# Optimization experiments

Measured on AMD Instinct MI355X. Metric: run time of the kernel, lower is better.

The kernel has to match this reference:

```python
import jax, jax.numpy as jnp
import numpy as np

LAMBDA = 0.5
WINDOW = 2
NUM_SCALES = 2
EPS = 1e-5


def setup_inputs() -> dict:
    key = jax.random.key(0)
    ks = jax.random.split(key, 9)
    N, C, T, Vw = 32, 96, 300, 50
    V = 25
    out_c = 192
    return {
        "x": jax.random.normal(ks[0], (N, C, T, Vw), jnp.float32),
        "xx": jax.random.normal(ks[1], (N, 3, 300, V), jnp.float32),
        "A_res": jax.random.normal(ks[2], (Vw, Vw), jnp.float32) * 1e-6,
        "W": jax.random.normal(ks[3], (out_c, NUM_SCALES * C), jnp.float32) * 0.05,
        "b": jax.random.normal(ks[4], (out_c,), jnp.float32) * 0.01,
        "gamma": jnp.ones((out_c,), jnp.float32),
        "beta": jnp.zeros((out_c,), jnp.float32),
        "running_mean": jax.random.normal(ks[5], (out_c,), jnp.float32) * 0.01,
        "running_var": jax.random.uniform(ks[6], (out_c,), jnp.float32, 0.5, 1.5),
    }


def reference(x, xx, A_res, W, b, gamma, beta, running_mean, running_var):
    # xx: (N, 3, 300, V) -> (N, T=300, V, C=3)
    xxp = jnp.transpose(xx, (0, 2, 3, 1))
    # pairwise squared L2 distances (norm then squared in exp == sum of squares)
    diff = xxp[:, :, :, None, :] - xxp[:, :, None, :, :]      # (N,T,V,V,3)
    dists2 = jnp.sum(diff * diff, axis=-1)                     # (N,T,V,V)
    A_dsg = jnp.exp(-dists2 / LAMBDA)
    # conv3d with (1,1,300,1,1) kernel of 1/300 == mean over the 300 frames
    A_t = jnp.mean(A_dsg, axis=1)                              # (N,V,V)
    # per-sample symmetric normalization D^-1/2 A D^-1/2
    deg = jnp.sum(A_t, axis=-1)                                # (N,V)
    dinv = deg ** -0.5
    A_norm = A_t * dinv[:, :, None] * dinv[:, None, :]
    # kron-style repeat to spatial-temporal graph (N, V*window, V*window)
    A_large = jnp.tile(A_norm, (1, WINDOW, WINDOW))
    A = A_large + A_res                                        # (N,Vw,Vw)
    # conv2d with (1,N,1,1) kernel of 1/N == mean over the batch
    A_scale = jnp.mean(A, axis=0)                              # (Vw,Vw)
    # graph conv
    agg = jnp.einsum('vu,nctu->nctv', A_scale, x)              # (N,C,T,Vw)
    N, C, T, Vw = x.shape
    Vs = Vw // NUM_SCALES
    agg = agg.reshape(N, C, T, NUM_SCALES, Vs)
    agg = jnp.transpose(agg, (0, 3, 1, 2, 4)).reshape(N, NUM_SCALES * C, T, Vs)
    # MLP: 1x1 conv + BN (activation='linear')
    out = jnp.einsum('oc,nctv->notv', W, agg) + b[None, :, None, None]
    scale = gamma * jax.lax.rsqrt(running_var + EPS)
    out = out * scale[None, :, None, None] + (beta - running_mean * scale)[None, :, None, None]
    return jax.nn.relu(out)
```

## Files before the change

### kernel.cpp

```cpp
#include <hip/hip_runtime.h>
#include <hip/hip_bf16.h>

typedef __attribute__((ext_vector_type(8))) short short8;
typedef __attribute__((ext_vector_type(4))) short short4v;
typedef __attribute__((ext_vector_type(4))) float f32x4;
typedef __attribute__((ext_vector_type(2))) float f32x2;

__device__ __forceinline__ unsigned short f2bf(float f) {
    unsigned int u = __builtin_bit_cast(unsigned int, f);
    u += 0x7fffu + ((u >> 16) & 1u);
    return (unsigned short)(u >> 16);
}
__device__ __forceinline__ unsigned int pack2(float a, float b) {
    union { __hip_bfloat162 h; unsigned int u; } r;
    r.h = __float22bfloat162_rn(make_float2(a, b));
    return r.u;
}
__device__ __forceinline__ short4v cvt4(float a, float b, float c, float d) {
    union { __hip_bfloat162 h[2]; short4v s; } u;
    u.h[0] = __float22bfloat162_rn(make_float2(a, b));
    u.h[1] = __float22bfloat162_rn(make_float2(c, d));
    return u.s;
}

__global__ void kA(const float* __restrict__ xx, float* __restrict__ At_part) {
    __shared__ float xs3[3][60][25];
    const int tc = blockIdx.x, n = blockIdx.y;
    const int tid = threadIdx.x;
    const float* base = xx + (size_t)n * 22500 + tc * 1500;
    for (int idx = tid; idx < 4500; idx += 256) {
        int ch = idx / 1500, rt = idx % 1500;
        xs3[ch][rt / 25][rt % 25] = base[ch * 7500 + rt];
    }
    __syncthreads();
    for (int p = tid; p < 625; p += 256) {
        int v = p / 25, u = p % 25;
        float s = 0.f;
        for (int t = 0; t < 60; ++t) {
            float dx = xs3[0][t][v] - xs3[0][t][u];
            float dy = xs3[1][t][v] - xs3[1][t][u];
            float dz = xs3[2][t][v] - xs3[2][t][u];
            s += __expf(-2.f * (dx * dx + dy * dy + dz * dz));
        }
        At_part[(size_t)(n * 5 + tc) * 625 + p] = s;
    }
}

__global__ void kB1(const float* __restrict__ At_part, float* __restrict__ Acontrib) {
    __shared__ float At[625];
    __shared__ float dinv[25];
    const int n = blockIdx.x, tid = threadIdx.x;
    for (int p = tid; p < 625; p += 256) {
        float s = 0.f;
        for (int tc = 0; tc < 5; ++tc) s += At_part[(size_t)(n * 5 + tc) * 625 + p];
        At[p] = s;
    }
    __syncthreads();
    if (tid < 25) {
        float d = 0.f;
        for (int u = 0; u < 25; ++u) d += At[tid * 25 + u];
        dinv[tid] = rsqrtf(d * (1.f / 300.f));
    }
    __syncthreads();
    for (int p = tid; p < 625; p += 256)
        Acontrib[n * 625 + p] = At[p] * (1.f / 300.f) * dinv[p / 25] * dinv[p % 25] * (1.f / 32.f);
}

__global__ void kB2(const float* __restrict__ Acontrib, const float* __restrict__ A_res,
                    const float* __restrict__ W, const float* __restrict__ b,
                    const float* __restrict__ gamma, const float* __restrict__ beta,
                    const float* __restrict__ rm, const float* __restrict__ rv,
                    short* __restrict__ bsTg, short* __restrict__ Wpg,
                    float* __restrict__ bbg) {
    const int tid = threadIdx.x;
    if (blockIdx.x == 0) {
        __shared__ float macc[625];
        for (int p = tid; p < 625; p += 256) {
            float s = 0.f;
            for (int n = 0; n < 32; ++n) s += Acontrib[n * 625 + p];
            macc[p] = s;
        }
        __syncthreads();
        for (int idx = tid; idx < 64 * 72; idx += 256) {
            int col = idx / 72, u = idx % 72;
            float v = 0.f;
            if (col < 50 && u < 50) v = macc[(col % 25) * 25 + (u % 25)] + A_res[col * 50 + u];
            bsTg[idx] = (short)f2bf(v);
        }
        if (tid < 192) {
            float sc = gamma[tid] * rsqrtf(rv[tid] + 1e-5f);
            bbg[tid] = b[tid] * sc + beta[tid] - rm[tid] * sc;
        }
    } else {
        const int e = (blockIdx.x - 1) * 1024 + tid * 4;
        const int o = e / 192;
        const float sc = gamma[o] * rsqrtf(rv[o] + 1e-5f);
        float4 w = *(const float4*)(W + e);
        short4v s4 = { (short)f2bf(w.x * sc), (short)f2bf(w.y * sc),
                       (short)f2bf(w.z * sc), (short)f2bf(w.w * sc) };
        *(short4v*)(Wpg + e) = s4;
    }
}

__global__ void kB2b(const float* __restrict__ W, const float* __restrict__ gamma,
                     const float* __restrict__ rv, short* __restrict__ Wfrag) {
    const int idx = blockIdx.x * 256 + threadIdx.x;
    const int ot = idx / 384, r = idx - ot * 384;
    const int ks = r / 64, lane = r - ks * 64;
    const int o = ot * 16 + (lane & 15);
    const int k0 = ks * 32 + (lane >> 4) * 8;
    const float sc = gamma[o] * rsqrtf(rv[o] + 1e-5f);
    float4 w0 = *(const float4*)(W + o * 192 + k0);
    float4 w1 = *(const float4*)(W + o * 192 + k0 + 4);
    union { short4v h[2]; short8 v; } u;
    u.h[0] = cvt4(w0.x * sc, w0.y * sc, w0.z * sc, w0.w * sc);
    u.h[1] = cvt4(w1.x * sc, w1.y * sc, w1.z * sc, w1.w * sc);
    *(short8*)(Wfrag + (size_t)idx * 8) = u.v;
}

__device__ __forceinline__ void ldx(const float* __restrict__ x, int gbase,
                                    f32x2 (&pf)[7], int tid) {
#pragma unroll
    for (int i = 0; i < 7; ++i) {
        int idx = i * 384 + tid;
        idx = idx < 2400 ? idx : 2399;
        int c = idx / 25, q = idx - c * 25;
        pf[i] = *(const f32x2*)(x + gbase + c * 15000 + 2 * q);
    }
}
__device__ __forceinline__ void stx(char* xsb, int slot, const f32x2 (&pf)[7], int tid) {
#pragma unroll
    for (int i = 0; i < 7; ++i) {
        int idx = i * 384 + tid;
        if (idx < 2400) {
            int c = idx / 25, q = idx - c * 25;
            *(unsigned int*)(xsb + ((slot * 12288 + c * 128 + q * 4) ^ ((c & 7) << 4)))
                = pack2(pf[i].x, pf[i].y);
        }
    }
}

__global__ __launch_bounds__(384, 3)
void kC(const float* __restrict__ x, const short* __restrict__ Wpg,
        const short* __restrict__ bsTg, const float* __restrict__ bbg,
        float* __restrict__ out) {
    __shared__ __align__(16) char xsb[2 * 12288];
    __shared__ __align__(16) short bsT[64 * 72];
    __shared__ __align__(16) short a2T[2][32][208];

    const int tid = threadIdx.x;
    const int lane = tid & 63;
    const int wid = tid >> 6;
    const int lam = lane & 15;
    const int kc = (lane >> 4) * 8;
    const int cb = (lane >> 4) * 4;
    const int n = blockIdx.y;
    const int t0 = blockIdx.x * 4;
    const int gb0 = n * 1440000 + t0 * 50;
    const int cgl = wid * 16 + lam;

    f32x2 pf2[13];
#pragma unroll
    for (int i = 0; i < 13; ++i) {
        int idx = i * 384 + tid;
        idx = idx < 4800 ? idx : 4799;
        int c = idx / 50, q2 = idx - c * 50;
        int tl = q2 >= 25, q = q2 - 25 * tl;
        pf2[i] = *(const f32x2*)(x + gb0 + c * 15000 + tl * 50 + 2 * q);
    }
    short8 wf[2][6];
#pragma unroll
    for (int ot = 0; ot < 2; ++ot)
#pragma unroll
        for (int ks = 0; ks < 6; ++ks)
            wf[ot][ks] = *(const short8*)(Wpg + ((2 * wid + ot) * 16 + lam) * 192 + ks * 32 + kc);
    float bb[2];
#pragma unroll
    for (int ot = 0; ot < 2; ++ot) bb[ot] = bbg[(2 * wid + ot) * 16 + lam];
    {
        const int4* src = (const int4*)bsTg;
        int4* dst = (int4*)bsT;
        for (int i = tid; i < 576; i += 384) dst[i] = src[i];
    }
    for (int idx = tid; idx < 1344; idx += 384) {
        int r = idx / 7, k = idx - r * 7;
        int slot = r / 96, c = r - 96 * slot;
        *(unsigned int*)(xsb + ((slot * 12288 + c * 128 + (50 + 2 * k) * 2) ^ ((c & 7) << 4))) = 0;
    }
    for (int idx = tid; idx < 1456; idx += 384) {
        int buf = idx / 728, rem = idx - buf * 728;
        int row = 25 + rem / 104, col2 = rem - (rem / 104) * 104;
        *((unsigned int*)&a2T[buf][row][0] + col2) = 0;
    }
#pragma unroll
    for (int i = 0; i < 13; ++i) {
        int idx = i * 384 + tid;
        if (idx < 4800) {
            int c = idx / 50, q2 = idx - c * 50;
            int tl = q2 >= 25, q = q2 - 25 * tl;
            *(unsigned int*)(xsb + ((tl * 12288 + c * 128 + q * 4) ^ ((c & 7) << 4)))
                = pack2(pf2[i].x, pf2[i].y);
        }
    }
    asm volatile("s_waitcnt lgkmcnt(0)" ::: "memory");
    __builtin_amdgcn_s_barrier();

    const f32x4 z = {0.f, 0.f, 0.f, 0.f};
    f32x2 pf[7];

#pragma unroll 1
    for (int tl = 0; tl < 4; ++tl) {
        const int slot = tl & 1;
        short* a2w = &a2T[slot][0][0];
        if (tl < 2) ldx(x, gb0 + (tl + 2) * 50, pf, tid);

        short8 xb[2];
#pragma unroll
        for (int ks = 0; ks < 2; ++ks)
            xb[ks] = *(const short8*)(xsb +
                ((slot * 12288 + cgl * 128 + (ks * 32 + kc) * 2) ^ ((cgl & 7) << 4)));
        f32x4 acc1[4];
#pragma unroll
        for (int m = 0; m < 4; ++m) acc1[m] = z;
#pragma unroll
        for (int ks = 0; ks < 2; ++ks)
#pragma unroll
            for (int m = 0; m < 4; ++m) {
                const short8 af = *(const short8*)(bsT + (m * 16 + lam) * 72 + ks * 32 + kc);
                acc1[m] = __builtin_amdgcn_mfma_f32_16x16x32_bf16(af, xb[ks], acc1[m], 0, 0, 0);
            }
#pragma unroll
        for (int m = 0; m < 3; ++m) {
            short4v sv = cvt4(acc1[m][0], acc1[m][1], acc1[m][2], acc1[m][3]);
#pragma unroll
            for (int r = 0; r < 4; ++r) {
                const int v = m * 16 + cb + r;
                const int s = v >= 25;
                a2w[(v - 25 * s) * 208 + s * 96 + cgl] = sv[r];
            }
        }
        if (cb == 0) {
            a2w[23 * 208 + 96 + cgl] = (short)f2bf(acc1[3][0]);
            a2w[24 * 208 + 96 + cgl] = (short)f2bf(acc1[3][1]);
        }
        asm volatile("s_waitcnt lgkmcnt(0)" ::: "memory");
        __builtin_amdgcn_s_barrier();

        f32x4 acc2[2][2];
#pragma unroll
        for (int g = 0; g < 2; ++g) { acc2[g][0] = z; acc2[g][1] = z; }
#pragma unroll
        for (int ks = 0; ks < 6; ++ks) {
            const short8 A0 = *(const short8*)(a2w + lam * 208 + ks * 32 + kc);
            const short8 A1 = *(const short8*)(a2w + (16 + lam) * 208 + ks * 32 + kc);
#pragma unroll
            for (int ot = 0; ot < 2; ++ot) {
                acc2[0][ot] = __builtin_amdgcn_mfma_f32_16x16x32_bf16(A0, wf[ot][ks], acc2[0][ot], 0, 0, 0);
                acc2[1][ot] = __builtin_amdgcn_mfma_f32_16x16x32_bf16(A1, wf[ot][ks], acc2[1][ot], 0, 0, 0);
            }
        }
        if (tl < 2) stx(xsb, slot, pf, tid);

        const int t = t0 + tl;
#pragma unroll
        for (int ot = 0; ot < 2; ++ot) {
            const int o = (2 * wid + ot) * 16 + lam;
            float* op = out + ((size_t)(n * 192 + o) * 300 + t) * 25;
#pragma unroll
            for (int r = 0; r < 4; ++r) {
                float vv = acc2[0][ot][r] + bb[ot];
                op[cb + r] = vv > 0.f ? vv : 0.f;
            }
#pragma unroll
            for (int r = 0; r < 4; ++r) {
                const int tv = 16 + cb + r;
                if (tv < 25) {
                    float vv = acc2[1][ot][r] + bb[ot];
                    op[tv] = vv > 0.f ? vv : 0.f;
                }
            }
        }
    }
}

__global__ __launch_bounds__(384, 3)
void kC1(const float* __restrict__ x, const short* __restrict__ bsTg,
         short* __restrict__ agg2) {
    __shared__ __align__(16) char xsb[2 * 12288];
    __shared__ __align__(16) short bsT[64 * 72];
    __shared__ __align__(16) short a2T[2][32][208];

    const int tid = threadIdx.x;
    const int lane = tid & 63;
    const int wid = tid >> 6;
    const int lam = lane & 15;
    const int kc = (lane >> 4) * 8;
    const int cb = (lane >> 4) * 4;
    const int n = blockIdx.y;
    const int t0 = blockIdx.x * 4;
    const int gb0 = n * 1440000 + t0 * 50;
    const int cgl = wid * 16 + lam;

    f32x2 pf2[13];
#pragma unroll
    for (int i = 0; i < 13; ++i) {
        int idx = i * 384 + tid;
        idx = idx < 4800 ? idx : 4799;
        int c = idx / 50, q2 = idx - c * 50;
        int tl = q2 >= 25, q = q2 - 25 * tl;
        pf2[i] = *(const f32x2*)(x + gb0 + c * 15000 + tl * 50 + 2 * q);
    }
    {
        const int4* src = (const int4*)bsTg;
        int4* dst = (int4*)bsT;
        for (int i = tid; i < 576; i += 384) dst[i] = src[i];
    }
    for (int idx = tid; idx < 1344; idx += 384) {
        int r = idx / 7, k = idx - r * 7;
        int slot = r / 96, c = r - 96 * slot;
        *(unsigned int*)(xsb + ((slot * 12288 + c * 128 + (50 + 2 * k) * 2) ^ ((c & 7) << 4))) = 0;
    }
#pragma unroll
    for (int i = 0; i < 13; ++i) {
        int idx = i * 384 + tid;
        if (idx < 4800) {
            int c = idx / 50, q2 = idx - c * 50;
            int tl = q2 >= 25, q = q2 - 25 * tl;
            *(unsigned int*)(xsb + ((tl * 12288 + c * 128 + q * 4) ^ ((c & 7) << 4)))
                = pack2(pf2[i].x, pf2[i].y);
        }
    }
    asm volatile("s_waitcnt lgkmcnt(0)" ::: "memory");
    __builtin_amdgcn_s_barrier();

    const f32x4 z = {0.f, 0.f, 0.f, 0.f};
    f32x2 pf[7];

#pragma unroll 1
    for (int tl = 0; tl < 4; ++tl) {
        const int slot = tl & 1;
        short* a2w = &a2T[slot][0][0];
        if (tl < 2) ldx(x, gb0 + (tl + 2) * 50, pf, tid);

        short8 xb[2];
#pragma unroll
        for (int ks = 0; ks < 2; ++ks)
            xb[ks] = *(const short8*)(xsb +
                ((slot * 12288 + cgl * 128 + (ks * 32 + kc) * 2) ^ ((cgl & 7) << 4)));
        f32x4 acc1[4];
#pragma unroll
        for (int m = 0; m < 4; ++m) acc1[m] = z;
#pragma unroll
        for (int ks = 0; ks < 2; ++ks)
#pragma unroll
            for (int m = 0; m < 4; ++m) {
                const short8 af = *(const short8*)(bsT + (m * 16 + lam) * 72 + ks * 32 + kc);
                acc1[m] = __builtin_amdgcn_mfma_f32_16x16x32_bf16(af, xb[ks], acc1[m], 0, 0, 0);
            }
#pragma unroll
        for (int m = 0; m < 3; ++m) {
            short4v sv = cvt4(acc1[m][0], acc1[m][1], acc1[m][2], acc1[m][3]);
#pragma unroll
            for (int r = 0; r < 4; ++r) {
                const int v = m * 16 + cb + r;
                const int s = v >= 25;
                a2w[(v - 25 * s) * 208 + s * 96 + cgl] = sv[r];
            }
        }
        if (cb == 0) {
            a2w[23 * 208 + 96 + cgl] = (short)f2bf(acc1[3][0]);
            a2w[24 * 208 + 96 + cgl] = (short)f2bf(acc1[3][1]);
        }
        asm volatile("s_waitcnt lgkmcnt(0)" ::: "memory");
        __builtin_amdgcn_s_barrier();

        {
            const unsigned int* a2d = (const unsigned int*)a2w;
            unsigned int* dst = (unsigned int*)agg2
                + (size_t)n * 720000 + (size_t)(t0 + tl) * 2400;
#pragma unroll
            for (int i = 0; i < 7; ++i) {
                int idx = i * 384 + tid;
                if (idx < 2400) {
                    int v = idx / 96, c2 = idx - v * 96;
                    dst[v * 96 + c2] = a2d[v * 104 + c2];
                }
            }
        }
        if (tl < 2) stx(xsb, slot, pf, tid);
    }
}

__global__ __launch_bounds__(256, 3)
void kC2(const short* __restrict__ agg2, const short* __restrict__ Wfrag,
         const float* __restrict__ bbg, float* __restrict__ out) {
    __shared__ __align__(16) unsigned int asb[64 * 100];

    const int tid = threadIdx.x;
    const int lane = tid & 63;
    const int wid = tid >> 6;
    const int lam = lane & 15;
    const int kc = (lane >> 4) * 8;
    const int cb = (lane >> 4) * 4;
    const int n = blockIdx.y;
    const int tv0 = blockIdx.x * 64;

    short8 wf[3][6];
    float bb[3];
#pragma unroll
    for (int j = 0; j < 3; ++j) {
        const int ot = wid * 3 + j;
#pragma unroll
        for (int ks = 0; ks < 6; ++ks)
            wf[j][ks] = *(const short8*)(Wfrag + ((size_t)(ot * 6 + ks) * 64 + lane) * 8);
        bb[j] = bbg[ot * 16 + lam];
    }

    {
        const unsigned int* src = (const unsigned int*)agg2 + (size_t)n * 720000;
#pragma unroll
        for (int k = 0; k < 24; ++k) {
            int d = k * 256 + tid;
            int row = d / 96, c2 = d - row * 96;
            int tvg = tv0 + row;
            tvg = tvg < 7500 ? tvg : 7499;
            asb[row * 100 + c2] = src[(size_t)tvg * 96 + c2];
        }
    }
    __syncthreads();

    const f32x4 z = {0.f, 0.f, 0.f, 0.f};
    f32x4 acc[4][3];
#pragma unroll
    for (int m = 0; m < 4; ++m)
#pragma unroll
        for (int j = 0; j < 3; ++j) acc[m][j] = z;

#pragma unroll
    for (int ks = 0; ks < 6; ++ks) {
        short8 a[4];
#pragma unroll
        for (int m = 0; m < 4; ++m)
            a[m] = *(const short8*)((const short*)asb + (m * 16 + lam) * 200 + ks * 32 + kc);
#pragma unroll
        for (int m = 0; m < 4; ++m)
#pragma unroll
            for (int j = 0; j < 3; ++j)
                acc[m][j] = __builtin_amdgcn_mfma_f32_16x16x32_bf16(a[m], wf[j][ks], acc[m][j], 0, 0, 0);
    }

#pragma unroll
    for (int m = 0; m < 4; ++m) {
        const int tvg = tv0 + m * 16 + cb;
        if (tvg < 7500) {
#pragma unroll
            for (int j = 0; j < 3; ++j) {
                const int o = (wid * 3 + j) * 16 + lam;
                float4 v;
                v.x = acc[m][j][0] + bb[j]; v.x = v.x > 0.f ? v.x : 0.f;
                v.y = acc[m][j][1] + bb[j]; v.y = v.y > 0.f ? v.y : 0.f;
                v.z = acc[m][j][2] + bb[j]; v.z = v.z > 0.f ? v.z : 0.f;
                v.w = acc[m][j][3] + bb[j]; v.w = v.w > 0.f ? v.w : 0.f;
                *(float4*)(out + (size_t)(n * 192 + o) * 7500 + tvg) = v;
            }
        }
    }
}

extern "C" void kernel_launch(void* const* d_in, const int* in_sizes, int n_in,
                              void* d_out, int out_size, void* d_ws, size_t ws_size,
                              hipStream_t stream) {
    const float* x     = (const float*)d_in[0];
    const float* xx    = (const float*)d_in[1];
    const float* A_res = (const float*)d_in[2];
    const float* W     = (const float*)d_in[3];
    const float* b     = (const float*)d_in[4];
    const float* gamma = (const float*)d_in[5];
    const float* beta  = (const float*)d_in[6];
    const float* rm    = (const float*)d_in[7];
    const float* rv    = (const float*)d_in[8];
    float* out = (float*)d_out;

    char* ws = (char*)d_ws;
    float* At_part  = (float*)ws;
    float* Acontrib = (float*)(ws + 400000);
    short* bsTg     = (short*)(ws + 480000);
    short* Wpg      = (short*)(ws + 489216);
    float* bbg      = (float*)(ws + 562944);
    short* Wfrag    = (short*)(ws + 563712);
    short* agg2     = (short*)(ws + 637440);
    const bool bigws = ws_size >= (size_t)637440 + 92160000u;

    kA<<<dim3(5, 32), 256, 0, stream>>>(xx, At_part);
    kB1<<<32, 256, 0, stream>>>(At_part, Acontrib);
    kB2<<<37, 256, 0, stream>>>(Acontrib, A_res, W, b, gamma, beta, rm, rv, bsTg, Wpg, bbg);
    kB2b<<<18, 256, 0, stream>>>(W, gamma, rv, Wfrag);

    if (bigws) {
        kC1<<<dim3(75, 32), 384, 0, stream>>>(x, bsTg, agg2);
        kC2<<<dim3(118, 32), 256, 0, stream>>>(agg2, Wfrag, bbg, out);
    } else {
        kC<<<dim3(75, 32), 384, 0, stream>>>(x, Wpg, bsTg, bbg, out);
    }
}
```

Baseline: 182.7 us.

## Process 20 frames per kC1 block and vectorize agg2 stores

Each kC1 block now handles 20 time frames instead of 4, cutting the grid from 75x32 to 15x32 blocks. Per-block setup (loading bsT, the first x prefetch, index math) is spread over more frames, and the gather/store offsets are precomputed into registers once. The agg2 copy-out now writes two 32-bit words per thread instead of one. The cost is fewer blocks in flight (480 total), which may underfill the GPU, plus higher register pressure from the offset arrays.

```diff
diff --git a/kernel.cpp b/kernel.cpp
--- a/kernel.cpp
+++ b/kernel.cpp
@@ -5,6 +5,7 @@
 typedef __attribute__((ext_vector_type(4))) short short4v;
 typedef __attribute__((ext_vector_type(4))) float f32x4;
 typedef __attribute__((ext_vector_type(2))) float f32x2;
+typedef __attribute__((ext_vector_type(2))) unsigned int u32x2;
 
 __device__ __forceinline__ unsigned short f2bf(float f) {
     unsigned int u = __builtin_bit_cast(unsigned int, f);
@@ -297,9 +298,26 @@
     const int kc = (lane >> 4) * 8;
     const int cb = (lane >> 4) * 4;
     const int n = blockIdx.y;
-    const int t0 = blockIdx.x * 4;
+    const int t0 = blockIdx.x * 20;
     const int gb0 = n * 1440000 + t0 * 50;
     const int cgl = wid * 16 + lam;
+
+    int goff[7], loff[7];
+#pragma unroll
+    for (int i = 0; i < 7; ++i) {
+        int idx = i * 384 + tid;
+        int idc = idx < 2400 ? idx : 2399;
+        int c = idc / 25, q = idc - c * 25;
+        goff[i] = c * 15000 + 2 * q;
+        loff[i] = (c * 128 + q * 4) ^ ((c & 7) << 4);
+    }
+    int asrc[4];
+#pragma unroll
+    for (int i = 0; i < 4; ++i) {
+        int idx = i * 768 + tid * 2;
+        int idc = idx < 2400 ? idx : 2398;
+        asrc[i] = idc + (idc / 96) * 8;
+    }
 
     f32x2 pf2[13];
 #pragma unroll
@@ -337,10 +355,16 @@
     f32x2 pf[7];
 
 #pragma unroll 1
-    for (int tl = 0; tl < 4; ++tl) {
+    for (int tl = 0; tl < 20; ++tl) {
         const int slot = tl & 1;
         short* a2w = &a2T[slot][0][0];
-        if (tl < 2) ldx(x, gb0 + (tl + 2) * 50, pf, tid);
+
+        if (tl < 18) {
+            const float* xb2 = x + gb0 + (tl + 2) * 50;
+#pragma unroll
+            for (int i = 0; i < 7; ++i)
+                if (i < 6 || tid < 96) pf[i] = *(const f32x2*)(xb2 + goff[i]);
+        }
 
         short8 xb[2];
 #pragma unroll
@@ -357,6 +381,7 @@
                 const short8 af = *(const short8*)(bsT + (m * 16 + lam) * 72 + ks * 32 + kc);
                 acc1[m] = __builtin_amdgcn_mfma_f32_16x16x32_bf16(af, xb[ks], acc1[m], 0, 0, 0);
             }
+
 #pragma unroll
         for (int m = 0; m < 3; ++m) {
             short4v sv = cvt4(acc1[m][0], acc1[m][1], acc1[m][2], acc1[m][3]);
@@ -379,15 +404,24 @@
             unsigned int* dst = (unsigned int*)agg2
                 + (size_t)n * 720000 + (size_t)(t0 + tl) * 2400;
 #pragma unroll
-            for (int i = 0; i < 7; ++i) {
-                int idx = i * 384 + tid;
-                if (idx < 2400) {
-                    int v = idx / 96, c2 = idx - v * 96;
-                    dst[v * 96 + c2] = a2d[v * 104 + c2];
+            for (int i = 0; i < 4; ++i) {
+                int idx = i * 768 + tid * 2;
+                if (i < 3 || tid < 48) {
+                    u32x2 v;
+                    v.x = a2d[asrc[i]];
+                    v.y = a2d[asrc[i] + 1];
+                    *(u32x2*)(dst + idx) = v;
                 }
             }
         }
-        if (tl < 2) stx(xsb, slot, pf, tid);
+
+        if (tl < 18) {
+            char* xw = xsb + slot * 12288;
+#pragma unroll
+            for (int i = 0; i < 7; ++i)
+                if (i < 6 || tid < 96)
+                    *(unsigned int*)(xw + loff[i]) = pack2(pf[i].x, pf[i].y);
+        }
     }
 }
 
@@ -497,7 +531,7 @@
     kB2b<<<18, 256, 0, stream>>>(W, gamma, rv, Wfrag);
 
     if (bigws) {
-        kC1<<<dim3(75, 32), 384, 0, stream>>>(x, bsTg, agg2);
+        kC1<<<dim3(15, 32), 384, 0, stream>>>(x, bsTg, agg2);
         kC2<<<dim3(118, 32), 256, 0, stream>>>(agg2, Wfrag, bbg, out);
     } else {
         kC<<<dim3(75, 32), 384, 0, stream>>>(x, Wpg, bsTg, bbg, out);
```

Result: faster. 167.4 us (-8.4%).

## Restructure graph-conv split: wave-local kC1 storing padded agg2, transpose in kC2

Applied to the files above, without the earlier changes.

kC1 now makes each wave own its 16 channels end to end: the first-stage MFMA fragments are kept in registers and the block barriers are dropped. It also processes 10 timesteps per block and writes the accumulator rows straight to global memory in a padded channel-major layout (64 shorts per channel). kC2 now works on 2 timesteps per block and does the vertex/scale transpose itself while staging into LDS, using scalar short stores. The aim is to remove the LDS transpose and barriers from kC1. In exchange, the intermediate grows by padding, the kC2 staging becomes scattered, and the larger workspace requirement may route execution to the fallback kernel.

```diff
diff --git a/kernel.cpp b/kernel.cpp
--- a/kernel.cpp
+++ b/kernel.cpp
@@ -118,8 +118,205 @@
     *(short8*)(Wfrag + (size_t)idx * 8) = u.v;
 }
 
-__device__ __forceinline__ void ldx(const float* __restrict__ x, int gbase,
-                                    f32x2 (&pf)[7], int tid) {
+#define TC1 10
+__global__ __launch_bounds__(384, 4)
+void kC1(const float* __restrict__ x, const short* __restrict__ bsTg,
+         short* __restrict__ agg2) {
+    __shared__ __align__(16) char xsb[2 * 12288];
+
+    const int tid = threadIdx.x;
+    const int lane = tid & 63;
+    const int wid = tid >> 6;
+    const int lam = lane & 15;
+    const int kc = (lane >> 4) * 8;
+    const int cb = (lane >> 4) * 4;
+    const int n = blockIdx.y;
+    const int t0 = blockIdx.x * TC1;
+    const int gb0 = n * 1440000 + t0 * 50;
+    const int cgl = wid * 16 + lam;
+
+    short8 af[2][4];
+#pragma unroll
+    for (int ks = 0; ks < 2; ++ks)
+#pragma unroll
+        for (int m = 0; m < 4; ++m)
+            af[ks][m] = *(const short8*)(bsTg + (m * 16 + lam) * 72 + ks * 32 + kc);
+
+    int goff[7], loff[7];
+#pragma unroll
+    for (int i = 0; i < 7; ++i) {
+        int idx = i * 64 + lane;
+        int idc = idx < 400 ? idx : 399;
+        int cl = idc / 25, q = idc - cl * 25;
+        int c = wid * 16 + cl;
+        goff[i] = c * 15000 + 2 * q;
+        loff[i] = (c * 128 + q * 4) ^ ((c & 7) << 4);
+    }
+
+#pragma unroll
+    for (int i = 0; i < 4; ++i) {
+        int idx = i * 64 + lane;
+        if (idx < 224) {
+            int slot = idx / 112, rem = idx - slot * 112;
+            int cl = rem / 7, k = rem - cl * 7;
+            int c = wid * 16 + cl;
+            *(unsigned int*)(xsb + slot * 12288 +
+                ((c * 128 + (50 + 2 * k) * 2) ^ ((c & 7) << 4))) = 0;
+        }
+    }
+
+    {
+        f32x2 p0[7], p1[7];
+#pragma unroll
+        for (int i = 0; i < 7; ++i) p0[i] = *(const f32x2*)(x + gb0 + goff[i]);
+#pragma unroll
+        for (int i = 0; i < 7; ++i) p1[i] = *(const f32x2*)(x + gb0 + 50 + goff[i]);
+#pragma unroll
+        for (int i = 0; i < 7; ++i)
+            if (i * 64 + lane < 400)
+                *(unsigned int*)(xsb + loff[i]) = pack2(p0[i].x, p0[i].y);
+#pragma unroll
+        for (int i = 0; i < 7; ++i)
+            if (i * 64 + lane < 400)
+                *(unsigned int*)(xsb + 12288 + loff[i]) = pack2(p1[i].x, p1[i].y);
+    }
+
+    const f32x4 z = {0.f, 0.f, 0.f, 0.f};
+    f32x2 pf[7];
+
+#pragma unroll 1
+    for (int tl = 0; tl < TC1; ++tl) {
+        const int slot = tl & 1;
+        const int t = t0 + tl;
+
+        if (tl < TC1 - 2) {
+            const float* xb2 = x + gb0 + (tl + 2) * 50;
+#pragma unroll
+            for (int i = 0; i < 7; ++i) pf[i] = *(const f32x2*)(xb2 + goff[i]);
+        }
+
+        short8 xb[2];
+#pragma unroll
+        for (int ks = 0; ks < 2; ++ks)
+            xb[ks] = *(const short8*)(xsb + slot * 12288 +
+                ((cgl * 128 + (ks * 32 + kc) * 2) ^ ((cgl & 7) << 4)));
+        f32x4 acc1[4];
+#pragma unroll
+        for (int m = 0; m < 4; ++m) acc1[m] = z;
+#pragma unroll
+        for (int ks = 0; ks < 2; ++ks)
+#pragma unroll
+            for (int m = 0; m < 4; ++m)
+                acc1[m] = __builtin_amdgcn_mfma_f32_16x16x32_bf16(af[ks][m], xb[ks], acc1[m], 0, 0, 0);
+
+        short* basep = agg2 + ((size_t)(n * 300 + t) * 96 + cgl) * 64;
+#pragma unroll
+        for (int m = 0; m < 3; ++m)
+            *(short4v*)(basep + m * 16 + cb) =
+                cvt4(acc1[m][0], acc1[m][1], acc1[m][2], acc1[m][3]);
+        if (cb == 0)
+            *(unsigned int*)(basep + 48) = pack2(acc1[3][0], acc1[3][1]);
+
+        if (tl < TC1 - 2) {
+#pragma unroll
+            for (int i = 0; i < 7; ++i)
+                if (i * 64 + lane < 400)
+                    *(unsigned int*)(xsb + slot * 12288 + loff[i]) = pack2(pf[i].x, pf[i].y);
+        }
+    }
+}
+
+__global__ __launch_bounds__(256, 3)
+void kC2(const short* __restrict__ agg2, const short* __restrict__ Wfrag,
+         const float* __restrict__ bbg, float* __restrict__ out) {
+    __shared__ __align__(16) short asb[64][208];
+
+    const int tid = threadIdx.x;
+    const int lane = tid & 63;
+    const int wid = tid >> 6;
+    const int lam = lane & 15;
+    const int kc = (lane >> 4) * 8;
+    const int cb = (lane >> 4) * 4;
+    const int n = blockIdx.y;
+    const int t0 = blockIdx.x * 2;
+
+    short8 wf[3][6];
+    float bb[3];
+#pragma unroll
+    for (int j = 0; j < 3; ++j) {
+        const int ot = wid * 3 + j;
+#pragma unroll
+        for (int ks = 0; ks < 6; ++ks)
+            wf[j][ks] = *(const short8*)(Wfrag + ((size_t)(ot * 6 + ks) * 64 + lane) * 8);
+        bb[j] = bbg[ot * 16 + lam];
+    }
+
+    for (int i = tid; i < 1456; i += 256) {
+        int r = 50 + i / 104, c2 = i - (i / 104) * 104;
+        *((unsigned int*)&asb[r][0] + c2) = 0;
+    }
+
+    {
+        const unsigned int* src = (const unsigned int*)agg2
+            + ((size_t)(n * 300 + t0) * 96) * 32;
+        for (int i = tid; i < 4800; i += 256) {
+            int tl = i / 2400, rem = i - tl * 2400;
+            int c = rem / 25, j = rem - c * 25;
+            unsigned int d = src[(tl * 96 + c) * 32 + j];
+            int v0 = 2 * j, v1 = 2 * j + 1;
+            int r0 = tl * 25 + (v0 >= 25 ? v0 - 25 : v0), s0 = (v0 >= 25) ? 96 : 0;
+            int r1 = tl * 25 + (v1 >= 25 ? v1 - 25 : v1), s1 = (v1 >= 25) ? 96 : 0;
+            asb[r0][s0 + c] = (short)(d & 0xffffu);
+            asb[r1][s1 + c] = (short)(d >> 16);
+        }
+    }
+    __syncthreads();
+
+    const f32x4 z = {0.f, 0.f, 0.f, 0.f};
+    f32x4 acc[4][3];
+#pragma unroll
+    for (int m = 0; m < 4; ++m)
+#pragma unroll
+        for (int j = 0; j < 3; ++j) acc[m][j] = z;
+
+#pragma unroll
+    for (int ks = 0; ks < 6; ++ks) {
+        short8 a[4];
+#pragma unroll
+        for (int m = 0; m < 4; ++m)
+            a[m] = *(const short8*)(&asb[m * 16 + lam][ks * 32 + kc]);
+#pragma unroll
+        for (int m = 0; m < 4; ++m)
+#pragma unroll
+            for (int j = 0; j < 3; ++j)
+                acc[m][j] = __builtin_amdgcn_mfma_f32_16x16x32_bf16(a[m], wf[j][ks], acc[m][j], 0, 0, 0);
+    }
+
+#pragma unroll
+    for (int m = 0; m < 4; ++m) {
+        const int tvb = m * 16 + cb;
+        if (tvb < 50) {
+#pragma unroll
+            for (int j = 0; j < 3; ++j) {
+                const int o = (wid * 3 + j) * 16 + lam;
+                float* op = out + (size_t)(n * 192 + o) * 7500 + t0 * 25 + tvb;
+                float v0 = acc[m][j][0] + bb[j]; v0 = v0 > 0.f ? v0 : 0.f;
+                float v1 = acc[m][j][1] + bb[j]; v1 = v1 > 0.f ? v1 : 0.f;
+                f32x2 p0 = {v0, v1};
+                *(f32x2*)op = p0;
+                if (tvb < 48) {
+                    float v2 = acc[m][j][2] + bb[j]; v2 = v2 > 0.f ? v2 : 0.f;
+                    float v3 = acc[m][j][3] + bb[j]; v3 = v3 > 0.f ? v3 : 0.f;
+                    f32x2 p1 = {v2, v3};
+                    *(f32x2*)(op + 2) = p1;
+                }
+            }
+        }
+    }
+}
+
+__device__ __forceinline__ void ldx_fb(const float* __restrict__ x, int gbase,
+                                       f32x2 (&pf)[7], int tid) {
 #pragma unroll
     for (int i = 0; i < 7; ++i) {
         int idx = i * 384 + tid;
@@ -128,7 +325,7 @@
         pf[i] = *(const f32x2*)(x + gbase + c * 15000 + 2 * q);
     }
 }
-__device__ __forceinline__ void stx(char* xsb, int slot, const f32x2 (&pf)[7], int tid) {
+__device__ __forceinline__ void stx_fb(char* xsb, int slot, const f32x2 (&pf)[7], int tid) {
 #pragma unroll
     for (int i = 0; i < 7; ++i) {
         int idx = i * 384 + tid;
@@ -212,7 +409,7 @@
     for (int tl = 0; tl < 4; ++tl) {
         const int slot = tl & 1;
         short* a2w = &a2T[slot][0][0];
-        if (tl < 2) ldx(x, gb0 + (tl + 2) * 50, pf, tid);
+        if (tl < 2) ldx_fb(x, gb0 + (tl + 2) * 50, pf, tid);
 
         short8 xb[2];
 #pragma unroll
@@ -259,7 +456,7 @@
                 acc2[1][ot] = __builtin_amdgcn_mfma_f32_16x16x32_bf16(A1, wf[ot][ks], acc2[1][ot], 0, 0, 0);
             }
         }
-        if (tl < 2) stx(xsb, slot, pf, tid);
+        if (tl < 2) stx_fb(xsb, slot, pf, tid);
 
         const int t = t0 + tl;
 #pragma unroll
@@ -278,190 +475,6 @@
                     float vv = acc2[1][ot][r] + bb[ot];
                     op[tv] = vv > 0.f ? vv : 0.f;
                 }
-            }
-        }
-    }
-}
-
-__global__ __launch_bounds__(384, 3)
-void kC1(const float* __restrict__ x, const short* __restrict__ bsTg,
-         short* __restrict__ agg2) {
-    __shared__ __align__(16) char xsb[2 * 12288];
-    __shared__ __align__(16) short bsT[64 * 72];
-    __shared__ __align__(16) short a2T[2][32][208];
-
-    const int tid = threadIdx.x;
-    const int lane = tid & 63;
-    const int wid = tid >> 6;
-    const int lam = lane & 15;
-    const int kc = (lane >> 4) * 8;
-    const int cb = (lane >> 4) * 4;
-    const int n = blockIdx.y;
-    const int t0 = blockIdx.x * 4;
-    const int gb0 = n * 1440000 + t0 * 50;
-    const int cgl = wid * 16 + lam;
-
-    f32x2 pf2[13];
-#pragma unroll
-    for (int i = 0; i < 13; ++i) {
-        int idx = i * 384 + tid;
-        idx = idx < 4800 ? idx : 4799;
-        int c = idx / 50, q2 = idx - c * 50;
-        int tl = q2 >= 25, q = q2 - 25 * tl;
-        pf2[i] = *(const f32x2*)(x + gb0 + c * 15000 + tl * 50 + 2 * q);
-    }
-    {
-        const int4* src = (const int4*)bsTg;
-        int4* dst = (int4*)bsT;
-        for (int i = tid; i < 576; i += 384) dst[i] = src[i];
-    }
-    for (int idx = tid; idx < 1344; idx += 384) {
-        int r = idx / 7, k = idx - r * 7;
-        int slot = r / 96, c = r - 96 * slot;
-        *(unsigned int*)(xsb + ((slot * 12288 + c * 128 + (50 + 2 * k) * 2) ^ ((c & 7) << 4))) = 0;
-    }
-#pragma unroll
-    for (int i = 0; i < 13; ++i) {
-        int idx = i * 384 + tid;
-        if (idx < 4800) {
-            int c = idx / 50, q2 = idx - c * 50;
-            int tl = q2 >= 25, q = q2 - 25 * tl;
-            *(unsigned int*)(xsb + ((tl * 12288 + c * 128 + q * 4) ^ ((c & 7) << 4)))
-                = pack2(pf2[i].x, pf2[i].y);
-        }
-    }
-    asm volatile("s_waitcnt lgkmcnt(0)" ::: "memory");
-    __builtin_amdgcn_s_barrier();
-
-    const f32x4 z = {0.f, 0.f, 0.f, 0.f};
-    f32x2 pf[7];
-
-#pragma unroll 1
-    for (int tl = 0; tl < 4; ++tl) {
-        const int slot = tl & 1;
-        short* a2w = &a2T[slot][0][0];
-        if (tl < 2) ldx(x, gb0 + (tl + 2) * 50, pf, tid);
-
-        short8 xb[2];
-#pragma unroll
-        for (int ks = 0; ks < 2; ++ks)
-            xb[ks] = *(const short8*)(xsb +
-                ((slot * 12288 + cgl * 128 + (ks * 32 + kc) * 2) ^ ((cgl & 7) << 4)));
-        f32x4 acc1[4];
-#pragma unroll
-        for (int m = 0; m < 4; ++m) acc1[m] = z;
-#pragma unroll
-        for (int ks = 0; ks < 2; ++ks)
-#pragma unroll
-            for (int m = 0; m < 4; ++m) {
-                const short8 af = *(const short8*)(bsT + (m * 16 + lam) * 72 + ks * 32 + kc);
-                acc1[m] = __builtin_amdgcn_mfma_f32_16x16x32_bf16(af, xb[ks], acc1[m], 0, 0, 0);
-            }
-#pragma unroll
-        for (int m = 0; m < 3; ++m) {
-            short4v sv = cvt4(acc1[m][0], acc1[m][1], acc1[m][2], acc1[m][3]);
-#pragma unroll
-            for (int r = 0; r < 4; ++r) {
-                const int v = m * 16 + cb + r;
-                const int s = v >= 25;
-                a2w[(v - 25 * s) * 208 + s * 96 + cgl] = sv[r];
-            }
-        }
-        if (cb == 0) {
-            a2w[23 * 208 + 96 + cgl] = (short)f2bf(acc1[3][0]);
-            a2w[24 * 208 + 96 + cgl] = (short)f2bf(acc1[3][1]);
-        }
-        asm volatile("s_waitcnt lgkmcnt(0)" ::: "memory");
-        __builtin_amdgcn_s_barrier();
-
-        {
-            const unsigned int* a2d = (const unsigned int*)a2w;
-            unsigned int* dst = (unsigned int*)agg2
-                + (size_t)n * 720000 + (size_t)(t0 + tl) * 2400;
-#pragma unroll
-            for (int i = 0; i < 7; ++i) {
-                int idx = i * 384 + tid;
-                if (idx < 2400) {
-                    int v = idx / 96, c2 = idx - v * 96;
-                    dst[v * 96 + c2] = a2d[v * 104 + c2];
-                }
-            }
-        }
-        if (tl < 2) stx(xsb, slot, pf, tid);
-    }
-}
-
-__global__ __launch_bounds__(256, 3)
-void kC2(const short* __restrict__ agg2, const short* __restrict__ Wfrag,
-         const float* __restrict__ bbg, float* __restrict__ out) {
-    __shared__ __align__(16) unsigned int asb[64 * 100];
-
-    const int tid = threadIdx.x;
-    const int lane = tid & 63;
-    const int wid = tid >> 6;
-    const int lam = lane & 15;
-    const int kc = (lane >> 4) * 8;
-    const int cb = (lane >> 4) * 4;
-    const int n = blockIdx.y;
-    const int tv0 = blockIdx.x * 64;
-
-    short8 wf[3][6];
-    float bb[3];
-#pragma unroll
-    for (int j = 0; j < 3; ++j) {
-        const int ot = wid * 3 + j;
-#pragma unroll
-        for (int ks = 0; ks < 6; ++ks)
-            wf[j][ks] = *(const short8*)(Wfrag + ((size_t)(ot * 6 + ks) * 64 + lane) * 8);
-        bb[j] = bbg[ot * 16 + lam];
-    }
-
-    {
-        const unsigned int* src = (const unsigned int*)agg2 + (size_t)n * 720000;
-#pragma unroll
-        for (int k = 0; k < 24; ++k) {
-            int d = k * 256 + tid;
-            int row = d / 96, c2 = d - row * 96;
-            int tvg = tv0 + row;
-            tvg = tvg < 7500 ? tvg : 7499;
-            asb[row * 100 + c2] = src[(size_t)tvg * 96 + c2];
-        }
-    }
-    __syncthreads();
-
-    const f32x4 z = {0.f, 0.f, 0.f, 0.f};
-    f32x4 acc[4][3];
-#pragma unroll
-    for (int m = 0; m < 4; ++m)
-#pragma unroll
-        for (int j = 0; j < 3; ++j) acc[m][j] = z;
-
-#pragma unroll
-    for (int ks = 0; ks < 6; ++ks) {
-        short8 a[4];
-#pragma unroll
-        for (int m = 0; m < 4; ++m)
-            a[m] = *(const short8*)((const short*)asb + (m * 16 + lam) * 200 + ks * 32 + kc);
-#pragma unroll
-        for (int m = 0; m < 4; ++m)
-#pragma unroll
-            for (int j = 0; j < 3; ++j)
-                acc[m][j] = __builtin_amdgcn_mfma_f32_16x16x32_bf16(a[m], wf[j][ks], acc[m][j], 0, 0, 0);
-    }
-
-#pragma unroll
-    for (int m = 0; m < 4; ++m) {
-        const int tvg = tv0 + m * 16 + cb;
-        if (tvg < 7500) {
-#pragma unroll
-            for (int j = 0; j < 3; ++j) {
-                const int o = (wid * 3 + j) * 16 + lam;
-                float4 v;
-                v.x = acc[m][j][0] + bb[j]; v.x = v.x > 0.f ? v.x : 0.f;
-                v.y = acc[m][j][1] + bb[j]; v.y = v.y > 0.f ? v.y : 0.f;
-                v.z = acc[m][j][2] + bb[j]; v.z = v.z > 0.f ? v.z : 0.f;
-                v.w = acc[m][j][3] + bb[j]; v.w = v.w > 0.f ? v.w : 0.f;
-                *(float4*)(out + (size_t)(n * 192 + o) * 7500 + tvg) = v;
             }
         }
     }
@@ -489,7 +502,7 @@
     float* bbg      = (float*)(ws + 562944);
     short* Wfrag    = (short*)(ws + 563712);
     short* agg2     = (short*)(ws + 637440);
-    const bool bigws = ws_size >= (size_t)637440 + 92160000u;
+    const bool bigws = ws_size >= (size_t)637440 + 117964800u;
 
     kA<<<dim3(5, 32), 256, 0, stream>>>(xx, At_part);
     kB1<<<32, 256, 0, stream>>>(At_part, Acontrib);
@@ -497,8 +510,8 @@
     kB2b<<<18, 256, 0, stream>>>(W, gamma, rv, Wfrag);
 
     if (bigws) {
-        kC1<<<dim3(75, 32), 384, 0, stream>>>(x, bsTg, agg2);
-        kC2<<<dim3(118, 32), 256, 0, stream>>>(agg2, Wfrag, bbg, out);
+        kC1<<<dim3(30, 32), 384, 0, stream>>>(x, bsTg, agg2);
+        kC2<<<dim3(150, 32), 256, 0, stream>>>(agg2, Wfrag, bbg, out);
     } else {
         kC<<<dim3(75, 32), 384, 0, stream>>>(x, Wpg, bsTg, bbg, out);
     }
```

Result: slower. 240.6 us (+31.7%).
